# Kernel optimization log

Hardware: AMD Instinct MI355X
Metric: run time of the kernel (lower is better)

Reference implementation:

```python
import jax, jax.numpy as jnp
import numpy as np

QBITS = 8
QP = float(2 ** (QBITS - 1) - 1)  # 127 for 8-bit symmetric quantization


def quant(x, K):
    # learned-scale symmetric uniform quantization (fake-quant / dequant),
    # straight-through estimator for gradients
    xc = jnp.clip(x / K, -1.0, 1.0)
    q = jnp.round(xc * QP) / QP
    return (xc + jax.lax.stop_gradient(q - xc)) * K


def setup_inputs() -> dict:
    key = jax.random.key(0)
    k0, k1, k2 = jax.random.split(key, 3)
    B, S, D, H = 64, 197, 768, 3072  # ViT-B/16: 197 tokens, d=768, mlp=3072
    hidden_state = jax.random.normal(k0, (B, S, D), jnp.float32)
    # xavier-uniform-like scale for weights
    W1 = jax.random.normal(k1, (H, D), jnp.float32) * np.float32(1.0 / np.sqrt(D))
    b1 = jnp.zeros((H,), jnp.float32)
    W2 = jax.random.normal(k2, (D, H), jnp.float32) * np.float32(1.0 / np.sqrt(H))
    b2 = jnp.zeros((D,), jnp.float32)
    # learned per-layer activation / weight scale factors (kmlp_* lists)
    ka1 = jnp.array([3.0], jnp.float32)
    kw1 = jnp.array([0.1], jnp.float32)
    ka2 = jnp.array([3.0], jnp.float32)
    kw2 = jnp.array([0.1], jnp.float32)
    return {"hidden_state": hidden_state, "W1": W1, "b1": b1, "W2": W2,
            "b2": b2, "ka1": ka1, "kw1": kw1, "ka2": ka2, "kw2": kw2}


def reference(hidden_state, W1, b1, W2, b2, ka1, kw1, ka2, kw2):
    # fc1: quantize activations with Ka, weights with Kw, then GEMM + bias
    h = jnp.einsum("bsd,hd->bsh", quant(hidden_state, ka1), quant(W1, kw1)) + b1
    h = jax.nn.gelu(h, approximate=False)  # F.gelu default = exact erf
    # dropout is identity in eval mode
    out = jnp.einsum("bsh,dh->bsd", quant(h, ka2), quant(W2, kw2)) + b2
    return out
```

## Files before the change

### kernel.cpp

```cpp
#include <hip/hip_runtime.h>
#include <stdint.h>


typedef __attribute__((ext_vector_type(4))) int i32x4;

static constexpr int MROWS = 12608;
static constexpr int MPAD  = 12672;
static constexpr int DDIM  = 768;
static constexpr int HDIM  = 3072;

__device__ __forceinline__ int quant_one(float x, float K) {
    float xc = x / K;
    xc = fminf(fmaxf(xc, -1.0f), 1.0f);
    return (int)rintf(xc * 127.0f);
}

__global__ void quant_kernel(const float* __restrict__ x, int8_t* __restrict__ q,
                             const float* __restrict__ kp, int nvalid4, int ntot4) {
    int i = blockIdx.x * 256 + threadIdx.x;
    if (i >= ntot4) return;
    int packed = 0;
    if (i < nvalid4) {
        float K = kp[0];
        float4 v = reinterpret_cast<const float4*>(x)[i];
        packed = (quant_one(v.x, K) & 255)
               | ((quant_one(v.y, K) & 255) << 8)
               | ((quant_one(v.z, K) & 255) << 16)
               | ((quant_one(v.w, K) & 255) << 24);
    }
    reinterpret_cast<int*>(q)[i] = packed;
}

__device__ __forceinline__ void load16_to_lds(const int8_t* g, int8_t* l) {
    __builtin_amdgcn_global_load_lds(
        (const __attribute__((address_space(1))) void*)g,
        (__attribute__((address_space(3))) void*)l, 16, 0, 0);
}

template<int KD, int ND, bool EPI1>
__global__ __launch_bounds__(256)
void gemm_i8_kernel(const int8_t* __restrict__ A, const int8_t* __restrict__ B,
                    int8_t* __restrict__ qout, float* __restrict__ fout,
                    const float* __restrict__ bias,
                    const float* __restrict__ kA, const float* __restrict__ kW,
                    const float* __restrict__ kQ) {
    __shared__ __align__(16) int8_t Asm[128 * 64];
    __shared__ __align__(16) int8_t Bsm[128 * 64];

    const int tid  = threadIdx.x;
    const int lane = tid & 63;
    const int wave = tid >> 6;
    const int wr   = wave >> 1;
    const int wc   = wave & 1;
    const int bm   = blockIdx.y * 128;
    const int bn   = blockIdx.x * 128;

    i32x4 acc[4][4] = {};

    const int srow = tid >> 2;
    const int scol = (tid & 3) << 4;
    const int8_t* gA = A + (size_t)(bm + srow) * KD + scol;
    const int8_t* gB = B + (size_t)(bn + srow) * KD + scol;

    const int fr = lane & 15;
    const int kc = (lane >> 4) << 4;
    const int aoff = (wr * 64 + fr) * 64 + kc;
    const int boff = (wc * 64 + fr) * 64 + kc;

    for (int kt = 0; kt < KD; kt += 64) {
        load16_to_lds(gA + kt,                  Asm + 16 * tid);
        load16_to_lds(gA + (size_t)64 * KD + kt, Asm + 4096 + 16 * tid);
        load16_to_lds(gB + kt,                  Bsm + 16 * tid);
        load16_to_lds(gB + (size_t)64 * KD + kt, Bsm + 4096 + 16 * tid);
        __syncthreads();

        i32x4 af[4], bf[4];
#pragma unroll
        for (int m = 0; m < 4; ++m)
            af[m] = *reinterpret_cast<const i32x4*>(Asm + aoff + m * 1024);
#pragma unroll
        for (int n = 0; n < 4; ++n)
            bf[n] = *reinterpret_cast<const i32x4*>(Bsm + boff + n * 1024);
#pragma unroll
        for (int m = 0; m < 4; ++m)
#pragma unroll
            for (int n = 0; n < 4; ++n)
                acc[m][n] = __builtin_amdgcn_mfma_i32_16x16x64_i8(af[m], bf[n], acc[m][n], 0, 0, 0);
        __syncthreads();
    }

    const float sAW = kA[0] * kW[0] * (1.0f / 16129.0f);
    float kq = 1.0f;
    if constexpr (EPI1) kq = kQ[0];

    const int row0 = bm + wr * 64 + ((lane >> 4) << 2);
    const int col0 = bn + wc * 64 + fr;
#pragma unroll
    for (int m = 0; m < 4; ++m) {
#pragma unroll
        for (int n = 0; n < 4; ++n) {
            const int col = col0 + n * 16;
            const float bv = bias[col];
#pragma unroll
            for (int j = 0; j < 4; ++j) {
                const int row = row0 + m * 16 + j;
                float h = (float)acc[m][n][j] * sAW + bv;
                if constexpr (EPI1) {
                    float g  = 0.5f * h * (1.0f + erff(h * 0.70710678118654752f));
                    float xc = fminf(fmaxf(g / kq, -1.0f), 1.0f);
                    qout[(size_t)row * ND + col] = (int8_t)(int)rintf(xc * 127.0f);
                } else {
                    if (row < MROWS)
                        fout[(size_t)row * ND + col] = h;
                }
            }
        }
    }
}

extern "C" void kernel_launch(void* const* d_in, const int* in_sizes, int n_in,
                              void* d_out, int out_size, void* d_ws, size_t ws_size,
                              hipStream_t stream) {
    const float* hidden = (const float*)d_in[0];
    const float* W1     = (const float*)d_in[1];
    const float* b1     = (const float*)d_in[2];
    const float* W2     = (const float*)d_in[3];
    const float* b2     = (const float*)d_in[4];
    const float* ka1    = (const float*)d_in[5];
    const float* kw1    = (const float*)d_in[6];
    const float* ka2    = (const float*)d_in[7];
    const float* kw2    = (const float*)d_in[8];
    float* out = (float*)d_out;

    int8_t* a8  = (int8_t*)d_ws;
    int8_t* w1q = a8  + (size_t)MPAD * DDIM;
    int8_t* w2q = w1q + (size_t)HDIM * DDIM;
    int8_t* h8  = w2q + (size_t)DDIM * HDIM;

    {
        int ntot4 = MPAD * DDIM / 4, nval4 = MROWS * DDIM / 4;
        quant_kernel<<<(ntot4 + 255) / 256, 256, 0, stream>>>(hidden, a8, ka1, nval4, ntot4);
    }
    {
        int n4 = HDIM * DDIM / 4;
        quant_kernel<<<(n4 + 255) / 256, 256, 0, stream>>>(W1, w1q, kw1, n4, n4);
        quant_kernel<<<(n4 + 255) / 256, 256, 0, stream>>>(W2, w2q, kw2, n4, n4);
    }

    gemm_i8_kernel<DDIM, HDIM, true>
        <<<dim3(HDIM / 128, MPAD / 128), 256, 0, stream>>>
        (a8, w1q, h8, nullptr, b1, ka1, kw1, ka2);

    gemm_i8_kernel<HDIM, DDIM, false>
        <<<dim3(DDIM / 128, MPAD / 128), 256, 0, stream>>>
        (h8, w2q, nullptr, out, b2, ka2, kw2, nullptr);
}
```

Before: 252.7 us.

## Double-buffer int8 GEMM LDS, swizzle layout, remap blocks per XCD, fuse quant kernels

The int8 MFMA GEMM now keeps two LDS buffers so the global-to-LDS load of the next K tile overlaps compute on the current one, cutting the number of barrier stalls. LDS columns are XOR-swizzled to reduce bank conflicts, workgroups are remapped to a 1D grid so adjacent tiles land on the same XCD for L2 reuse, and MFMA sections get raised wave priority. The three quantization launches are merged into one. LDS use doubles, which may limit occupancy despite the launch-bounds hint.

```diff
diff --git a/kernel.cpp b/kernel.cpp
--- a/kernel.cpp
+++ b/kernel.cpp
@@ -15,85 +15,137 @@
     return (int)rintf(xc * 127.0f);
 }
 
-__global__ void quant_kernel(const float* __restrict__ x, int8_t* __restrict__ q,
-                             const float* __restrict__ kp, int nvalid4, int ntot4) {
+__global__ void quant_fused_kernel(const float* __restrict__ x,
+                                   const float* __restrict__ w1,
+                                   const float* __restrict__ w2,
+                                   int8_t* __restrict__ a8,
+                                   int8_t* __restrict__ w1q,
+                                   int8_t* __restrict__ w2q,
+                                   const float* __restrict__ ka1,
+                                   const float* __restrict__ kw1,
+                                   const float* __restrict__ kw2) {
+    constexpr int G1 = MPAD * DDIM / 4;
+    constexpr int GV = MROWS * DDIM / 4;
+    constexpr int G2 = HDIM * DDIM / 4;
     int i = blockIdx.x * 256 + threadIdx.x;
-    if (i >= ntot4) return;
+    const float4* src; int* dst; float K; int idx; bool valid = true;
+    if (i < G1) {
+        idx = i;           src = (const float4*)x;  dst = (int*)a8;  K = ka1[0];
+        valid = i < GV;
+    } else if (i < G1 + G2) {
+        idx = i - G1;      src = (const float4*)w1; dst = (int*)w1q; K = kw1[0];
+    } else if (i < G1 + 2 * G2) {
+        idx = i - G1 - G2; src = (const float4*)w2; dst = (int*)w2q; K = kw2[0];
+    } else return;
     int packed = 0;
-    if (i < nvalid4) {
-        float K = kp[0];
-        float4 v = reinterpret_cast<const float4*>(x)[i];
+    if (valid) {
+        float4 v = src[idx];
         packed = (quant_one(v.x, K) & 255)
                | ((quant_one(v.y, K) & 255) << 8)
                | ((quant_one(v.z, K) & 255) << 16)
                | ((quant_one(v.w, K) & 255) << 24);
     }
-    reinterpret_cast<int*>(q)[i] = packed;
-}
-
-__device__ __forceinline__ void load16_to_lds(const int8_t* g, int8_t* l) {
+    dst[idx] = packed;
+}
+
+__device__ __forceinline__ void load16_to_lds(const int8_t* g, const int8_t* l) {
     __builtin_amdgcn_global_load_lds(
         (const __attribute__((address_space(1))) void*)g,
         (__attribute__((address_space(3))) void*)l, 16, 0, 0);
 }
 
 template<int KD, int ND, bool EPI1>
-__global__ __launch_bounds__(256)
+__global__ __launch_bounds__(256, 3)
 void gemm_i8_kernel(const int8_t* __restrict__ A, const int8_t* __restrict__ B,
                     int8_t* __restrict__ qout, float* __restrict__ fout,
                     const float* __restrict__ bias,
                     const float* __restrict__ kA, const float* __restrict__ kW,
                     const float* __restrict__ kQ) {
-    __shared__ __align__(16) int8_t Asm[128 * 64];
-    __shared__ __align__(16) int8_t Bsm[128 * 64];
+    __shared__ __align__(16) int8_t As0[128 * 64];
+    __shared__ __align__(16) int8_t Bs0[128 * 64];
+    __shared__ __align__(16) int8_t As1[128 * 64];
+    __shared__ __align__(16) int8_t Bs1[128 * 64];
 
     const int tid  = threadIdx.x;
     const int lane = tid & 63;
     const int wave = tid >> 6;
     const int wr   = wave >> 1;
     const int wc   = wave & 1;
-    const int bm   = blockIdx.y * 128;
-    const int bn   = blockIdx.x * 128;
+
+    constexpr int NXB = ND / 128;
+    const int nwg = gridDim.x;
+    const int q   = nwg >> 3, r = nwg & 7;
+    const int xcd = blockIdx.x & 7, loc = blockIdx.x >> 3;
+    const int nb  = (xcd < r ? xcd * (q + 1) : r * (q + 1) + (xcd - r) * q) + loc;
+    const int bm  = (nb / NXB) * 128;
+    const int bn  = (nb % NXB) * 128;
 
     i32x4 acc[4][4] = {};
 
     const int srow = tid >> 2;
-    const int scol = (tid & 3) << 4;
-    const int8_t* gA = A + (size_t)(bm + srow) * KD + scol;
-    const int8_t* gB = B + (size_t)(bn + srow) * KD + scol;
+    const int soff = (((tid & 3) ^ ((tid >> 3) & 3)) << 4);
+    const int8_t* gA = A + (size_t)(bm + srow) * KD + soff;
+    const int8_t* gB = B + (size_t)(bn + srow) * KD + soff;
+    const int ldst = tid * 16;
+
+#define STAGE(LA, LB, ktb)                                                     \
+    do {                                                                       \
+        const int8_t* a_ = gA + (ktb);                                         \
+        const int8_t* b_ = gB + (ktb);                                         \
+        load16_to_lds(a_,                   LA + ldst);                        \
+        load16_to_lds(a_ + (size_t)64 * KD, LA + 4096 + ldst);                 \
+        load16_to_lds(b_,                   LB + ldst);                        \
+        load16_to_lds(b_ + (size_t)64 * KD, LB + 4096 + ldst);                 \
+    } while (0)
 
     const int fr = lane & 15;
-    const int kc = (lane >> 4) << 4;
-    const int aoff = (wr * 64 + fr) * 64 + kc;
-    const int boff = (wc * 64 + fr) * 64 + kc;
-
-    for (int kt = 0; kt < KD; kt += 64) {
-        load16_to_lds(gA + kt,                  Asm + 16 * tid);
-        load16_to_lds(gA + (size_t)64 * KD + kt, Asm + 4096 + 16 * tid);
-        load16_to_lds(gB + kt,                  Bsm + 16 * tid);
-        load16_to_lds(gB + (size_t)64 * KD + kt, Bsm + 4096 + 16 * tid);
+    const int q4 = lane >> 4;
+    const int cs = ((q4 ^ ((fr >> 1) & 3)) << 4);
+    int aoff[4], boff[4];
+#pragma unroll
+    for (int m = 0; m < 4; ++m) aoff[m] = (wr * 64 + m * 16 + fr) * 64 + cs;
+#pragma unroll
+    for (int n = 0; n < 4; ++n) boff[n] = (wc * 64 + n * 16 + fr) * 64 + cs;
+
+#define COMPUTE(LA, LB)                                                        \
+    do {                                                                       \
+        i32x4 af[4], bf[4];                                                    \
+        _Pragma("unroll")                                                      \
+        for (int m = 0; m < 4; ++m)                                            \
+            af[m] = *reinterpret_cast<const i32x4*>(LA + aoff[m]);             \
+        _Pragma("unroll")                                                      \
+        for (int n = 0; n < 4; ++n)                                            \
+            bf[n] = *reinterpret_cast<const i32x4*>(LB + boff[n]);             \
+        __builtin_amdgcn_s_setprio(1);                                         \
+        _Pragma("unroll")                                                      \
+        for (int m = 0; m < 4; ++m)                                            \
+            _Pragma("unroll")                                                  \
+            for (int n = 0; n < 4; ++n)                                        \
+                acc[m][n] = __builtin_amdgcn_mfma_i32_16x16x64_i8(             \
+                    af[m], bf[n], acc[m][n], 0, 0, 0);                         \
+        __builtin_amdgcn_s_setprio(0);                                         \
+    } while (0)
+
+    constexpr int NT = KD / 64;
+    STAGE(As0, Bs0, 0);
+    __syncthreads();
+
+    for (int t = 0; t < NT; t += 2) {
+        STAGE(As1, Bs1, (t + 1) * 64);
+        COMPUTE(As0, Bs0);
         __syncthreads();
-
-        i32x4 af[4], bf[4];
-#pragma unroll
-        for (int m = 0; m < 4; ++m)
-            af[m] = *reinterpret_cast<const i32x4*>(Asm + aoff + m * 1024);
-#pragma unroll
-        for (int n = 0; n < 4; ++n)
-            bf[n] = *reinterpret_cast<const i32x4*>(Bsm + boff + n * 1024);
-#pragma unroll
-        for (int m = 0; m < 4; ++m)
-#pragma unroll
-            for (int n = 0; n < 4; ++n)
-                acc[m][n] = __builtin_amdgcn_mfma_i32_16x16x64_i8(af[m], bf[n], acc[m][n], 0, 0, 0);
+        if (t + 2 < NT) STAGE(As0, Bs0, (t + 2) * 64);
+        COMPUTE(As1, Bs1);
         __syncthreads();
     }
+#undef STAGE
+#undef COMPUTE
 
     const float sAW = kA[0] * kW[0] * (1.0f / 16129.0f);
     float kq = 1.0f;
     if constexpr (EPI1) kq = kQ[0];
 
-    const int row0 = bm + wr * 64 + ((lane >> 4) << 2);
+    const int row0 = bm + wr * 64 + (q4 << 2);
     const int col0 = bn + wc * 64 + fr;
 #pragma unroll
     for (int m = 0; m < 4; ++m) {
@@ -138,20 +190,16 @@
     int8_t* h8  = w2q + (size_t)DDIM * HDIM;
 
     {
-        int ntot4 = MPAD * DDIM / 4, nval4 = MROWS * DDIM / 4;
-        quant_kernel<<<(ntot4 + 255) / 256, 256, 0, stream>>>(hidden, a8, ka1, nval4, ntot4);
-    }
-    {
-        int n4 = HDIM * DDIM / 4;
-        quant_kernel<<<(n4 + 255) / 256, 256, 0, stream>>>(W1, w1q, kw1, n4, n4);
-        quant_kernel<<<(n4 + 255) / 256, 256, 0, stream>>>(W2, w2q, kw2, n4, n4);
+        constexpr int GTOT = (MPAD * DDIM + 2 * HDIM * DDIM) / 4;
+        quant_fused_kernel<<<(GTOT + 255) / 256, 256, 0, stream>>>(
+            hidden, W1, W2, a8, w1q, w2q, ka1, kw1, kw2);
     }
 
     gemm_i8_kernel<DDIM, HDIM, true>
-        <<<dim3(HDIM / 128, MPAD / 128), 256, 0, stream>>>
+        <<<(HDIM / 128) * (MPAD / 128), 256, 0, stream>>>
         (a8, w1q, h8, nullptr, b1, ka1, kw1, ka2);
 
     gemm_i8_kernel<HDIM, DDIM, false>
-        <<<dim3(DDIM / 128, MPAD / 128), 256, 0, stream>>>
+        <<<(DDIM / 128) * (MPAD / 128), 256, 0, stream>>>
         (h8, w2q, nullptr, out, b2, ka2, kw2, nullptr);
 }
```

Result: faster. 225.4 us (-10.8%).
